# Optimization experiments

Measured on AMD Instinct MI355X. Metric: run time of the kernel, lower is better.

Reference implementation:

```python
import jax, jax.numpy as jnp
import numpy as np

HIDDEN = 128

def _conv1d(x, w, b):
    # x: [B, Cin, W], w: [Cout, Cin, K] (OIW), 'same' padding
    pad = w.shape[-1] // 2
    y = jax.lax.conv_general_dilated(
        x, w, window_strides=(1,), padding=[(pad, pad)],
        dimension_numbers=('NCH', 'OIH', 'NCH'))
    return y + b[None, :, None]

def setup_inputs() -> dict:
    key = jax.random.key(0)
    k1, k2, k3 = jax.random.split(key, 3)
    B, T, C, W = 16, 64, 64, 256
    K = 5
    fan_in = (C + HIDDEN) * K
    x = jax.random.normal(k1, (B, T, C, W), dtype=jnp.float32)
    W_conv = jax.random.normal(k2, (4 * HIDDEN, C + HIDDEN, K), dtype=jnp.float32) / np.sqrt(fan_in)
    b_conv = jax.random.normal(k3, (4 * HIDDEN,), dtype=jnp.float32) * 0.01
    return {"x": x, "W_conv": W_conv, "b_conv": b_conv}

def reference(x, W_conv, b_conv):
    B, T, C, W = x.shape
    h0 = jnp.zeros((B, HIDDEN, W), dtype=x.dtype)
    c0 = jnp.zeros((B, HIDDEN, W), dtype=x.dtype)

    def step(carry, xt):
        h, c = carry
        combined = jnp.concatenate([xt, h], axis=1)  # [B, C+H, W]
        conv_out = _conv1d(combined, W_conv, b_conv)  # [B, 4H, W]
        cc_i, cc_f, cc_o, cc_g = jnp.split(conv_out, 4, axis=1)
        i = jax.nn.sigmoid(cc_i)
        f = jax.nn.sigmoid(cc_f)
        o = jax.nn.sigmoid(cc_o)
        g = jnp.tanh(cc_g)
        c_next = f * c + i * g
        h_next = o * jnp.tanh(c_next)
        return (h_next, c_next), h_next

    xs = jnp.transpose(x, (1, 0, 2, 3))  # [T, B, C, W]
    (h, c), hs = jax.lax.scan(step, (h0, c0), xs)
    outputs = jnp.transpose(hs, (1, 0, 2, 3))  # [B, T, H, W]
    return outputs, h, c
```

## Files before the change

kernel.cpp:

```cpp
#include <hip/hip_runtime.h>
#include <hip/hip_bf16.h>
#include <math.h>

#define B_ 16
#define T_ 64
#define C_ 64
#define W_ 256
#define H_ 128
#define CH_ 192
#define K_ 5

#define OUT_SEQ_ELEMS ((size_t)B_ * T_ * H_ * W_)
#define OUT_H_OFF     OUT_SEQ_ELEMS
#define OUT_C_OFF     (OUT_SEQ_ELEMS + (size_t)B_ * H_ * W_)

#define WS_WF_OFF  0
#define WS_XT_OFF  (983040)
#define WS_HT_OFF  (WS_XT_OFF + 33554432)
#define WS_CNT_OFF (WS_HT_OFF + 2 * 1048576)

typedef __attribute__((ext_vector_type(8))) short bf16x8;
typedef __attribute__((ext_vector_type(4))) float f32x4;
typedef __attribute__((ext_vector_type(4))) unsigned int u32x4;

__device__ __forceinline__ float sigmoid_f(float x) {
    return 1.0f / (1.0f + __expf(-x));
}
__device__ __forceinline__ float tanh_f(float x) {
    return 1.0f - 2.0f / (__expf(2.0f * x) + 1.0f);
}

__global__ __launch_bounds__(256)
void prep_wfrag(const float* __restrict__ Wc, __hip_bfloat16* __restrict__ wf) {
    int idx = blockIdx.x * 256 + threadIdx.x;
    if (idx >= 960 * 64) return;
    int lane  = idx & 63;
    int f     = idx >> 6;
    int chunk = f % 6;
    int ktap  = (f / 6) % 5;
    int g     = (f / 30) % 4;
    int ht    = f / 120;
    int chan  = g * 128 + ht * 16 + (lane & 15);
    int ci0   = chunk * 32 + 8 * (lane >> 4);
    __hip_bfloat16 tmp[8];
#pragma unroll
    for (int j = 0; j < 8; ++j)
        tmp[j] = __float2bfloat16(Wc[((size_t)chan * CH_ + (ci0 + j)) * K_ + ktap]);
    *reinterpret_cast<u32x4*>(&wf[(size_t)idx * 8]) = *reinterpret_cast<const u32x4*>(tmp);
}

__global__ __launch_bounds__(256)
void prep_xt(const float* __restrict__ x, __hip_bfloat16* __restrict__ xt) {
    __shared__ float tile[64][65];
    int bt = blockIdx.x;
    int w0 = blockIdx.y * 64;
    const float* src = x + (size_t)bt * C_ * W_ + w0;
#pragma unroll
    for (int i = 0; i < 16; ++i) {
        int idx = i * 256 + threadIdx.x;
        int ci = idx >> 6, wr = idx & 63;
        tile[ci][wr] = src[(size_t)ci * W_ + wr];
    }
    __syncthreads();
    __hip_bfloat16* dst = xt + ((size_t)bt * W_ + w0) * C_;
#pragma unroll
    for (int i = 0; i < 8; ++i) {
        int idx = i * 256 + threadIdx.x;
        int wr = idx >> 5, cp = (idx & 31) * 2;
        __hip_bfloat16 a = __float2bfloat16(tile[cp][wr]);
        __hip_bfloat16 b = __float2bfloat16(tile[cp + 1][wr]);
        ushort2 v;
        v.x = *reinterpret_cast<unsigned short*>(&a);
        v.y = *reinterpret_cast<unsigned short*>(&b);
        *reinterpret_cast<ushort2*>(&dst[(size_t)wr * C_ + cp]) = v;
    }
}

__global__ void init_cnt(unsigned int* cnt) {
    if (threadIdx.x < 16 * 16) cnt[threadIdx.x] = 0;
}

#define PITCH_B 384
#define NROWS   132
#define GBUF_OFF 50688
#define HBF_OFF  (50688 + 32768)

__global__ __launch_bounds__(256, 1)
void lstm_persistent(const __hip_bfloat16* __restrict__ xt,
                     const __hip_bfloat16* __restrict__ wf,
                     const float* __restrict__ bc,
                     __hip_bfloat16* __restrict__ hbuf0,
                     __hip_bfloat16* __restrict__ hbuf1,
                     float* __restrict__ out,
                     unsigned int* __restrict__ cnt)
{
    __shared__ char lds[89600];
    const int ht   = blockIdx.x;
    const int wseg = blockIdx.y;
    const int b    = blockIdx.z;
    const int tid  = threadIdx.x;
    const int lane = tid & 63;
    const int g    = tid >> 6;
    const int l15  = lane & 15;
    const int lg   = lane >> 4;
    unsigned int* cntb = cnt + b * 16;

    bf16x8 wreg[30];
    {
        const __hip_bfloat16* wfbase = wf + (size_t)(ht * 4 + g) * 30 * 512 + (size_t)lane * 8;
#pragma unroll
        for (int f = 0; f < 30; ++f)
            wreg[f] = *reinterpret_cast<const bf16x8*>(wfbase + (size_t)f * 512);
    }
    float bias[4];
    {
        int chanbase = g * 128 + ht * 16 + (lg << 2);
#pragma unroll
        for (int r = 0; r < 4; ++r) bias[r] = bc[chanbase + r];
    }
    float cstate[8];
#pragma unroll
    for (int i = 0; i < 8; ++i) cstate[i] = 0.0f;

    const int wbase = wseg * 128 - 2;
    const int cib = 16 * lg;

    for (int idx = tid; idx < NROWS * 16; idx += 256) {
        int wrel = idx >> 4;
        int c16  = (idx & 15) + 8;
        int byteoff = wrel * PITCH_B + ((c16 * 16) ^ ((wrel & 7) << 4));
        u32x4 z = {0u, 0u, 0u, 0u};
        *reinterpret_cast<u32x4*>(lds + byteoff) = z;
    }

    for (int t = 0; t < T_; ++t) {
        const __hip_bfloat16* xrow = xt + ((size_t)(b * T_ + t) * W_) * C_;
        const __hip_bfloat16* hrow = ((t & 1) ? hbuf0 : hbuf1) + (size_t)b * W_ * H_;
        __hip_bfloat16* hout = ((t & 1) ? hbuf1 : hbuf0);

        for (int idx = tid; idx < NROWS * 8; idx += 256) {
            int wrel = idx >> 3;
            int c16  = idx & 7;
            int w = wbase + wrel;
            u32x4 v = {0u, 0u, 0u, 0u};
            if (w >= 0 && w < W_)
                v = *reinterpret_cast<const u32x4*>(xrow + (size_t)w * C_ + c16 * 8);
            int byteoff = wrel * PITCH_B + ((c16 * 16) ^ ((wrel & 7) << 4));
            *reinterpret_cast<u32x4*>(lds + byteoff) = v;
        }

        if (t > 0) {
            if (tid == 0) {
                unsigned int target = 16u * (unsigned int)t;
                while (__hip_atomic_load(cntb, __ATOMIC_RELAXED, __HIP_MEMORY_SCOPE_AGENT) < target)
                    __builtin_amdgcn_s_sleep(1);
            }
        }
        __syncthreads();
        __atomic_signal_fence(__ATOMIC_SEQ_CST);

        u32x4 hv[8];
        u32x4 hv8 = {0u, 0u, 0u, 0u};
        if (t > 0) {
            const u32x4 zz = {0u, 0u, 0u, 0u};
#pragma unroll
            for (int i = 0; i < 8; ++i) {
                int idx  = i * 256 + tid;
                int wrel = idx >> 4;
                int c16  = idx & 15;
                int w = wbase + wrel;
                hv[i] = zz;
                if (w >= 0 && w < W_) {
                    const __hip_bfloat16* hp = hrow + (size_t)w * H_ + c16 * 8;
                    asm volatile("global_load_dwordx4 %0, %1, off sc1"
                                 : "+v"(hv[i]) : "v"(hp));
                }
            }
            if (tid < 64) {
                int idx  = 2048 + tid;
                int wrel = idx >> 4;
                int c16  = idx & 15;
                int w = wbase + wrel;
                if (w >= 0 && w < W_) {
                    const __hip_bfloat16* hp = hrow + (size_t)w * H_ + c16 * 8;
                    asm volatile("global_load_dwordx4 %0, %1, off sc1"
                                 : "+v"(hv8) : "v"(hp));
                }
            }
        }

        f32x4 acc[8];
#pragma unroll
        for (int nf = 0; nf < 8; ++nf) {
            acc[nf][0] = bias[0]; acc[nf][1] = bias[1];
            acc[nf][2] = bias[2]; acc[nf][3] = bias[3];
        }
#pragma unroll
        for (int c = 0; c < 2; ++c) {
#pragma unroll
            for (int k = 0; k < K_; ++k) {
                bf16x8 afrag = wreg[k * 6 + c];
#pragma unroll
                for (int nf = 0; nf < 8; ++nf) {
                    int wrel = nf * 16 + l15 + k;
                    int byteoff = wrel * PITCH_B + ((c * 64 + cib) ^ ((wrel & 7) << 4));
                    bf16x8 bfrag = *reinterpret_cast<const bf16x8*>(lds + byteoff);
                    acc[nf] = __builtin_amdgcn_mfma_f32_16x16x32_bf16(afrag, bfrag, acc[nf], 0, 0, 0);
                }
            }
        }

        if (t > 0) {
            asm volatile("s_waitcnt vmcnt(0)" ::: "memory");
            __builtin_amdgcn_sched_barrier(0);
#pragma unroll
            for (int i = 0; i < 8; ++i) {
                int idx  = i * 256 + tid;
                int wrel = idx >> 4;
                int c16  = (idx & 15) + 8;
                int byteoff = wrel * PITCH_B + ((c16 * 16) ^ ((wrel & 7) << 4));
                *reinterpret_cast<u32x4*>(lds + byteoff) = hv[i];
            }
            if (tid < 64) {
                int idx  = 2048 + tid;
                int wrel = idx >> 4;
                int c16  = (idx & 15) + 8;
                int byteoff = wrel * PITCH_B + ((c16 * 16) ^ ((wrel & 7) << 4));
                *reinterpret_cast<u32x4*>(lds + byteoff) = hv8;
            }
        }
        __syncthreads();

#pragma unroll
        for (int c = 2; c < 6; ++c) {
#pragma unroll
            for (int k = 0; k < K_; ++k) {
                bf16x8 afrag = wreg[k * 6 + c];
#pragma unroll
                for (int nf = 0; nf < 8; ++nf) {
                    int wrel = nf * 16 + l15 + k;
                    int byteoff = wrel * PITCH_B + ((c * 64 + cib) ^ ((wrel & 7) << 4));
                    bf16x8 bfrag = *reinterpret_cast<const bf16x8*>(lds + byteoff);
                    acc[nf] = __builtin_amdgcn_mfma_f32_16x16x32_bf16(afrag, bfrag, acc[nf], 0, 0, 0);
                }
            }
        }

        float* gbuf = reinterpret_cast<float*>(lds + GBUF_OFF);
        {
            int rowb = lg << 2;
#pragma unroll
            for (int nf = 0; nf < 8; ++nf)
#pragma unroll
                for (int r = 0; r < 4; ++r)
                    gbuf[(g * 16 + rowb + r) * 128 + nf * 16 + l15] = acc[nf][r];
        }
        __syncthreads();

        __hip_bfloat16* hbf = reinterpret_cast<__hip_bfloat16*>(lds + HBF_OFF);
        float hn_r[8];
#pragma unroll
        for (int i = 0; i < 8; ++i) {
            int idx  = i * 256 + tid;
            int chan = idx >> 7;
            int pos  = idx & 127;
            float vi = gbuf[(0 * 16 + chan) * 128 + pos];
            float vf = gbuf[(1 * 16 + chan) * 128 + pos];
            float vo = gbuf[(2 * 16 + chan) * 128 + pos];
            float vg = gbuf[(3 * 16 + chan) * 128 + pos];
            float ii = sigmoid_f(vi), ff = sigmoid_f(vf), oo = sigmoid_f(vo), gg = tanh_f(vg);
            float cn = ff * cstate[i] + ii * gg;
            cstate[i] = cn;
            float hn = oo * tanh_f(cn);
            hn_r[i] = hn;
            hbf[pos * 24 + chan] = __float2bfloat16(hn);
        }
        __syncthreads();

        {
            int w = tid >> 1, grp = tid & 1;
            u32x4 v = *reinterpret_cast<const u32x4*>(lds + HBF_OFF + w * 48 + grp * 16);
            __hip_bfloat16* hp = hout + ((size_t)b * W_ + wseg * 128 + w) * H_ + ht * 16 + grp * 8;
            asm volatile("global_store_dwordx4 %0, %1, off sc1" :: "v"(hp), "v"(v) : "memory");
        }
        asm volatile("s_waitcnt vmcnt(0)" ::: "memory");
        __syncthreads();
        if (tid == 0)
            __hip_atomic_fetch_add(cntb, 1u, __ATOMIC_RELAXED, __HIP_MEMORY_SCOPE_AGENT);

        float* hw = out + ((size_t)(b * T_ + t) * H_ + ht * 16) * W_ + wseg * 128;
#pragma unroll
        for (int i = 0; i < 8; ++i) {
            int idx  = i * 256 + tid;
            int chan = idx >> 7;
            int pos  = idx & 127;
            hw[(size_t)chan * W_ + pos] = hn_r[i];
        }
        if (t == T_ - 1) {
#pragma unroll
            for (int i = 0; i < 8; ++i) {
                int idx  = i * 256 + tid;
                int chan = idx >> 7;
                int pos  = idx & 127;
                out[OUT_H_OFF + ((size_t)b * H_ + ht * 16 + chan) * W_ + wseg * 128 + pos] = hn_r[i];
                out[OUT_C_OFF + ((size_t)b * H_ + ht * 16 + chan) * W_ + wseg * 128 + pos] = cstate[i];
            }
        }
    }
}

extern "C" void kernel_launch(void* const* d_in, const int* in_sizes, int n_in,
                              void* d_out, int out_size, void* d_ws, size_t ws_size,
                              hipStream_t stream)
{
    const float* x  = (const float*)d_in[0];
    const float* Wc = (const float*)d_in[1];
    const float* bc = (const float*)d_in[2];
    float* out = (float*)d_out;
    char*  ws  = (char*)d_ws;

    __hip_bfloat16* wf  = (__hip_bfloat16*)(ws + WS_WF_OFF);
    __hip_bfloat16* xt  = (__hip_bfloat16*)(ws + WS_XT_OFF);
    __hip_bfloat16* hb0 = (__hip_bfloat16*)(ws + WS_HT_OFF);
    __hip_bfloat16* hb1 = (__hip_bfloat16*)(ws + WS_HT_OFF + 1048576);
    unsigned int*   cnt = (unsigned int*)(ws + WS_CNT_OFF);

    prep_wfrag<<<240, 256, 0, stream>>>(Wc, wf);
    prep_xt<<<dim3(B_ * T_, 4), 256, 0, stream>>>(x, xt);
    init_cnt<<<1, 256, 0, stream>>>(cnt);

    lstm_persistent<<<dim3(8, 2, B_), 256, 0, stream>>>(xt, wf, bc, hb0, hb1, out, cnt);
}
```

Baseline: 791.8 us.

## Split warps by gate pair and width half; prefetch next x-step into separate LDS region

Each warp now owns two gates and half of the width positions instead of one gate across all positions, so each B-fragment loaded from LDS feeds two MFMAs. This halves LDS fragment reads per MFMA, at the cost of twice as many weight registers (60 bf16x8 fragments per thread). The x and h tiles move to separate LDS regions with their own pitches. The next timestep's x tile is loaded while the kernel waits on the inter-block h barrier, taking the x load off the critical path. The extra register pressure risks spills or lower scheduling freedom.

```diff
diff --git a/kernel.cpp b/kernel.cpp
--- a/kernel.cpp
+++ b/kernel.cpp
@@ -80,8 +80,11 @@
     if (threadIdx.x < 16 * 16) cnt[threadIdx.x] = 0;
 }
 
-#define PITCH_B 384
 #define NROWS   132
+#define XPITCH  128
+#define HPITCH  256
+#define XOFF    0
+#define HOFF    16896
 #define GBUF_OFF 50688
 #define HBF_OFF  (50688 + 32768)
 
@@ -100,23 +103,28 @@
     const int b    = blockIdx.z;
     const int tid  = threadIdx.x;
     const int lane = tid & 63;
-    const int g    = tid >> 6;
+    const int wid  = tid >> 6;
+    const int gp   = wid & 1;
+    const int nh   = wid >> 1;
     const int l15  = lane & 15;
     const int lg   = lane >> 4;
     unsigned int* cntb = cnt + b * 16;
 
-    bf16x8 wreg[30];
-    {
-        const __hip_bfloat16* wfbase = wf + (size_t)(ht * 4 + g) * 30 * 512 + (size_t)lane * 8;
+    bf16x8 wreg[2][30];
+#pragma unroll
+    for (int gl = 0; gl < 2; ++gl) {
+        const __hip_bfloat16* wfbase =
+            wf + (size_t)(ht * 4 + 2 * gp + gl) * 30 * 512 + (size_t)lane * 8;
 #pragma unroll
         for (int f = 0; f < 30; ++f)
-            wreg[f] = *reinterpret_cast<const bf16x8*>(wfbase + (size_t)f * 512);
-    }
-    float bias[4];
-    {
-        int chanbase = g * 128 + ht * 16 + (lg << 2);
-#pragma unroll
-        for (int r = 0; r < 4; ++r) bias[r] = bc[chanbase + r];
+            wreg[gl][f] = *reinterpret_cast<const bf16x8*>(wfbase + (size_t)f * 512);
+    }
+    float bias[2][4];
+#pragma unroll
+    for (int gl = 0; gl < 2; ++gl) {
+        int chanbase = (2 * gp + gl) * 128 + ht * 16 + (lg << 2);
+#pragma unroll
+        for (int r = 0; r < 4; ++r) bias[gl][r] = bc[chanbase + r];
     }
     float cstate[8];
 #pragma unroll
@@ -125,28 +133,70 @@
     const int wbase = wseg * 128 - 2;
     const int cib = 16 * lg;
 
-    for (int idx = tid; idx < NROWS * 16; idx += 256) {
-        int wrel = idx >> 4;
-        int c16  = (idx & 15) + 8;
-        int byteoff = wrel * PITCH_B + ((c16 * 16) ^ ((wrel & 7) << 4));
-        u32x4 z = {0u, 0u, 0u, 0u};
-        *reinterpret_cast<u32x4*>(lds + byteoff) = z;
-    }
-
-    for (int t = 0; t < T_; ++t) {
-        const __hip_bfloat16* xrow = xt + ((size_t)(b * T_ + t) * W_) * C_;
-        const __hip_bfloat16* hrow = ((t & 1) ? hbuf0 : hbuf1) + (size_t)b * W_ * H_;
-        __hip_bfloat16* hout = ((t & 1) ? hbuf1 : hbuf0);
-
+    {
+        const __hip_bfloat16* xrow0 = xt + ((size_t)(b * T_ + 0) * W_) * C_;
         for (int idx = tid; idx < NROWS * 8; idx += 256) {
             int wrel = idx >> 3;
             int c16  = idx & 7;
             int w = wbase + wrel;
             u32x4 v = {0u, 0u, 0u, 0u};
             if (w >= 0 && w < W_)
-                v = *reinterpret_cast<const u32x4*>(xrow + (size_t)w * C_ + c16 * 8);
-            int byteoff = wrel * PITCH_B + ((c16 * 16) ^ ((wrel & 7) << 4));
+                v = *reinterpret_cast<const u32x4*>(xrow0 + (size_t)w * C_ + c16 * 8);
+            int byteoff = XOFF + wrel * XPITCH + ((c16 * 16) ^ ((wrel & 7) << 4));
             *reinterpret_cast<u32x4*>(lds + byteoff) = v;
+        }
+        for (int idx = tid; idx < NROWS * 16; idx += 256) {
+            int wrel = idx >> 4;
+            int slot = idx & 15;
+            int byteoff = HOFF + wrel * HPITCH + ((slot * 16) ^ ((wrel & 7) << 4));
+            u32x4 z = {0u, 0u, 0u, 0u};
+            *reinterpret_cast<u32x4*>(lds + byteoff) = z;
+        }
+    }
+    __syncthreads();
+
+    for (int t = 0; t < T_; ++t) {
+        const __hip_bfloat16* hrow = ((t & 1) ? hbuf0 : hbuf1) + (size_t)b * W_ * H_;
+        __hip_bfloat16* hout = ((t & 1) ? hbuf1 : hbuf0);
+
+        f32x4 acc[2][4];
+#pragma unroll
+        for (int gl = 0; gl < 2; ++gl)
+#pragma unroll
+            for (int nf = 0; nf < 4; ++nf) {
+                acc[gl][nf][0] = bias[gl][0]; acc[gl][nf][1] = bias[gl][1];
+                acc[gl][nf][2] = bias[gl][2]; acc[gl][nf][3] = bias[gl][3];
+            }
+#pragma unroll
+        for (int c = 0; c < 2; ++c)
+#pragma unroll
+            for (int k = 0; k < K_; ++k) {
+#pragma unroll
+                for (int nf = 0; nf < 4; ++nf) {
+                    int wrel = (nh * 4 + nf) * 16 + l15 + k;
+                    int byteoff = XOFF + wrel * XPITCH +
+                                  ((c * 64 + cib) ^ ((wrel & 7) << 4));
+                    bf16x8 bfrag = *reinterpret_cast<const bf16x8*>(lds + byteoff);
+                    acc[0][nf] = __builtin_amdgcn_mfma_f32_16x16x32_bf16(
+                        wreg[0][k * 6 + c], bfrag, acc[0][nf], 0, 0, 0);
+                    acc[1][nf] = __builtin_amdgcn_mfma_f32_16x16x32_bf16(
+                        wreg[1][k * 6 + c], bfrag, acc[1][nf], 0, 0, 0);
+                }
+            }
+        __syncthreads();
+
+        if (t + 1 < T_) {
+            const __hip_bfloat16* xrow = xt + ((size_t)(b * T_ + t + 1) * W_) * C_;
+            for (int idx = tid; idx < NROWS * 8; idx += 256) {
+                int wrel = idx >> 3;
+                int c16  = idx & 7;
+                int w = wbase + wrel;
+                u32x4 v = {0u, 0u, 0u, 0u};
+                if (w >= 0 && w < W_)
+                    v = *reinterpret_cast<const u32x4*>(xrow + (size_t)w * C_ + c16 * 8);
+                int byteoff = XOFF + wrel * XPITCH + ((c16 * 16) ^ ((wrel & 7) << 4));
+                *reinterpret_cast<u32x4*>(lds + byteoff) = v;
+            }
         }
 
         if (t > 0) {
@@ -159,19 +209,19 @@
         __syncthreads();
         __atomic_signal_fence(__ATOMIC_SEQ_CST);
 
-        u32x4 hv[8];
-        u32x4 hv8 = {0u, 0u, 0u, 0u};
         if (t > 0) {
+            u32x4 hv[8];
+            u32x4 hv8 = {0u, 0u, 0u, 0u};
             const u32x4 zz = {0u, 0u, 0u, 0u};
 #pragma unroll
             for (int i = 0; i < 8; ++i) {
                 int idx  = i * 256 + tid;
                 int wrel = idx >> 4;
-                int c16  = idx & 15;
+                int slot = idx & 15;
                 int w = wbase + wrel;
                 hv[i] = zz;
                 if (w >= 0 && w < W_) {
-                    const __hip_bfloat16* hp = hrow + (size_t)w * H_ + c16 * 8;
+                    const __hip_bfloat16* hp = hrow + (size_t)w * H_ + slot * 8;
                     asm volatile("global_load_dwordx4 %0, %1, off sc1"
                                  : "+v"(hv[i]) : "v"(hp));
                 }
@@ -179,81 +229,65 @@
             if (tid < 64) {
                 int idx  = 2048 + tid;
                 int wrel = idx >> 4;
-                int c16  = idx & 15;
+                int slot = idx & 15;
                 int w = wbase + wrel;
                 if (w >= 0 && w < W_) {
-                    const __hip_bfloat16* hp = hrow + (size_t)w * H_ + c16 * 8;
+                    const __hip_bfloat16* hp = hrow + (size_t)w * H_ + slot * 8;
                     asm volatile("global_load_dwordx4 %0, %1, off sc1"
                                  : "+v"(hv8) : "v"(hp));
                 }
             }
-        }
-
-        f32x4 acc[8];
-#pragma unroll
-        for (int nf = 0; nf < 8; ++nf) {
-            acc[nf][0] = bias[0]; acc[nf][1] = bias[1];
-            acc[nf][2] = bias[2]; acc[nf][3] = bias[3];
-        }
-#pragma unroll
-        for (int c = 0; c < 2; ++c) {
-#pragma unroll
-            for (int k = 0; k < K_; ++k) {
-                bf16x8 afrag = wreg[k * 6 + c];
-#pragma unroll
-                for (int nf = 0; nf < 8; ++nf) {
-                    int wrel = nf * 16 + l15 + k;
-                    int byteoff = wrel * PITCH_B + ((c * 64 + cib) ^ ((wrel & 7) << 4));
-                    bf16x8 bfrag = *reinterpret_cast<const bf16x8*>(lds + byteoff);
-                    acc[nf] = __builtin_amdgcn_mfma_f32_16x16x32_bf16(afrag, bfrag, acc[nf], 0, 0, 0);
-                }
-            }
-        }
-
-        if (t > 0) {
             asm volatile("s_waitcnt vmcnt(0)" ::: "memory");
             __builtin_amdgcn_sched_barrier(0);
 #pragma unroll
             for (int i = 0; i < 8; ++i) {
                 int idx  = i * 256 + tid;
                 int wrel = idx >> 4;
-                int c16  = (idx & 15) + 8;
-                int byteoff = wrel * PITCH_B + ((c16 * 16) ^ ((wrel & 7) << 4));
+                int slot = idx & 15;
+                int byteoff = HOFF + wrel * HPITCH + ((slot * 16) ^ ((wrel & 7) << 4));
                 *reinterpret_cast<u32x4*>(lds + byteoff) = hv[i];
             }
             if (tid < 64) {
                 int idx  = 2048 + tid;
                 int wrel = idx >> 4;
-                int c16  = (idx & 15) + 8;
-                int byteoff = wrel * PITCH_B + ((c16 * 16) ^ ((wrel & 7) << 4));
+                int slot = idx & 15;
+                int byteoff = HOFF + wrel * HPITCH + ((slot * 16) ^ ((wrel & 7) << 4));
                 *reinterpret_cast<u32x4*>(lds + byteoff) = hv8;
             }
         }
         __syncthreads();
 
 #pragma unroll
-        for (int c = 2; c < 6; ++c) {
+        for (int c = 2; c < 6; ++c)
 #pragma unroll
             for (int k = 0; k < K_; ++k) {
-                bf16x8 afrag = wreg[k * 6 + c];
-#pragma unroll
-                for (int nf = 0; nf < 8; ++nf) {
-                    int wrel = nf * 16 + l15 + k;
-                    int byteoff = wrel * PITCH_B + ((c * 64 + cib) ^ ((wrel & 7) << 4));
+#pragma unroll
+                for (int nf = 0; nf < 4; ++nf) {
+                    int wrel = (nh * 4 + nf) * 16 + l15 + k;
+                    int byteoff = HOFF + wrel * HPITCH +
+                                  (((c - 2) * 64 + cib) ^ ((wrel & 7) << 4));
                     bf16x8 bfrag = *reinterpret_cast<const bf16x8*>(lds + byteoff);
-                    acc[nf] = __builtin_amdgcn_mfma_f32_16x16x32_bf16(afrag, bfrag, acc[nf], 0, 0, 0);
-                }
-            }
-        }
+                    acc[0][nf] = __builtin_amdgcn_mfma_f32_16x16x32_bf16(
+                        wreg[0][k * 6 + c], bfrag, acc[0][nf], 0, 0, 0);
+                    acc[1][nf] = __builtin_amdgcn_mfma_f32_16x16x32_bf16(
+                        wreg[1][k * 6 + c], bfrag, acc[1][nf], 0, 0, 0);
+                }
+            }
 
         float* gbuf = reinterpret_cast<float*>(lds + GBUF_OFF);
         {
             int rowb = lg << 2;
 #pragma unroll
-            for (int nf = 0; nf < 8; ++nf)
-#pragma unroll
-                for (int r = 0; r < 4; ++r)
-                    gbuf[(g * 16 + rowb + r) * 128 + nf * 16 + l15] = acc[nf][r];
+            for (int gl = 0; gl < 2; ++gl) {
+                int grow = (2 * gp + gl) * 16 + rowb;
+#pragma unroll
+                for (int nf = 0; nf < 4; ++nf) {
+                    int col = (nh * 4 + nf) * 16 + l15;
+#pragma unroll
+                    for (int r = 0; r < 4; ++r)
+                        gbuf[(grow + r) * 128 + col] = acc[gl][nf][r];
+                }
+            }
         }
         __syncthreads();
 
```

New measurement: 816.3 us. 1.03x slower.

## Replace atomic counter barrier with per-block flag slots and register-packed h store

Applied to the files above, without the earlier changes.

Each block now publishes its completed timestep to its own padded flag slot instead of incrementing a shared per-batch counter. Waiters poll all 16 slots in parallel across a wavefront. The gate epilogue is remapped so each thread owns 8 channels at one position, which lets it pack bf16 h values in registers and store them directly, removing the LDS staging buffer and one __syncthreads. The gate buffer also gets an XOR swizzle to cut LDS bank conflicts. The cost is that each thread's fp32 output writes now stride across channels.

```diff
diff --git a/kernel.cpp b/kernel.cpp
--- a/kernel.cpp
+++ b/kernel.cpp
@@ -77,13 +77,13 @@
 }
 
 __global__ void init_cnt(unsigned int* cnt) {
-    if (threadIdx.x < 16 * 16) cnt[threadIdx.x] = 0;
+    cnt[blockIdx.x * 256 + threadIdx.x] = 0;
 }
 
 #define PITCH_B 384
 #define NROWS   132
 #define GBUF_OFF 50688
-#define HBF_OFF  (50688 + 32768)
+#define GIDX2(row, col) ((row) * 128 + ((col) ^ ((((row) >> 2) & 3) << 4)))
 
 __global__ __launch_bounds__(256, 1)
 void lstm_persistent(const __hip_bfloat16* __restrict__ xt,
@@ -92,18 +92,19 @@
                      __hip_bfloat16* __restrict__ hbuf0,
                      __hip_bfloat16* __restrict__ hbuf1,
                      float* __restrict__ out,
-                     unsigned int* __restrict__ cnt)
+                     unsigned int* __restrict__ slots)
 {
-    __shared__ char lds[89600];
+    __shared__ char lds[83456];
     const int ht   = blockIdx.x;
     const int wseg = blockIdx.y;
     const int b    = blockIdx.z;
+    const int hw16 = ht * 2 + wseg;
     const int tid  = threadIdx.x;
     const int lane = tid & 63;
     const int g    = tid >> 6;
     const int l15  = lane & 15;
     const int lg   = lane >> 4;
-    unsigned int* cntb = cnt + b * 16;
+    unsigned int* slotb = slots + (size_t)b * 256;
 
     bf16x8 wreg[30];
     {
@@ -118,12 +119,11 @@
 #pragma unroll
         for (int r = 0; r < 4; ++r) bias[r] = bc[chanbase + r];
     }
+    const int epos = tid & 127;
+    const int ehi  = tid >> 7;
     float cstate[8];
 #pragma unroll
     for (int i = 0; i < 8; ++i) cstate[i] = 0.0f;
-
-    const int wbase = wseg * 128 - 2;
-    const int cib = 16 * lg;
 
     for (int idx = tid; idx < NROWS * 16; idx += 256) {
         int wrel = idx >> 4;
@@ -132,6 +132,9 @@
         u32x4 z = {0u, 0u, 0u, 0u};
         *reinterpret_cast<u32x4*>(lds + byteoff) = z;
     }
+
+    const int wbase = wseg * 128 - 2;
+    const int cib = 16 * lg;
 
     for (int t = 0; t < T_; ++t) {
         const __hip_bfloat16* xrow = xt + ((size_t)(b * T_ + t) * W_) * C_;
@@ -149,12 +152,12 @@
             *reinterpret_cast<u32x4*>(lds + byteoff) = v;
         }
 
-        if (t > 0) {
-            if (tid == 0) {
-                unsigned int target = 16u * (unsigned int)t;
-                while (__hip_atomic_load(cntb, __ATOMIC_RELAXED, __HIP_MEMORY_SCOPE_AGENT) < target)
-                    __builtin_amdgcn_s_sleep(1);
-            }
+        if (t > 0 && tid < 64) {
+            unsigned int tgt = (unsigned int)t;
+            const unsigned int* sp = slotb + (lane & 15) * 16;
+            while (!__all(__hip_atomic_load(sp, __ATOMIC_RELAXED,
+                                            __HIP_MEMORY_SCOPE_AGENT) >= tgt))
+                __builtin_amdgcn_s_sleep(1);
         }
         __syncthreads();
         __atomic_signal_fence(__ATOMIC_SEQ_CST);
@@ -167,11 +170,11 @@
             for (int i = 0; i < 8; ++i) {
                 int idx  = i * 256 + tid;
                 int wrel = idx >> 4;
-                int c16  = idx & 15;
+                int slot = idx & 15;
                 int w = wbase + wrel;
                 hv[i] = zz;
                 if (w >= 0 && w < W_) {
-                    const __hip_bfloat16* hp = hrow + (size_t)w * H_ + c16 * 8;
+                    const __hip_bfloat16* hp = hrow + (size_t)w * H_ + slot * 8;
                     asm volatile("global_load_dwordx4 %0, %1, off sc1"
                                  : "+v"(hv[i]) : "v"(hp));
                 }
@@ -179,10 +182,10 @@
             if (tid < 64) {
                 int idx  = 2048 + tid;
                 int wrel = idx >> 4;
-                int c16  = idx & 15;
+                int slot = idx & 15;
                 int w = wbase + wrel;
                 if (w >= 0 && w < W_) {
-                    const __hip_bfloat16* hp = hrow + (size_t)w * H_ + c16 * 8;
+                    const __hip_bfloat16* hp = hrow + (size_t)w * H_ + slot * 8;
                     asm volatile("global_load_dwordx4 %0, %1, off sc1"
                                  : "+v"(hv8) : "v"(hp));
                 }
@@ -252,58 +255,54 @@
 #pragma unroll
             for (int nf = 0; nf < 8; ++nf)
 #pragma unroll
-                for (int r = 0; r < 4; ++r)
-                    gbuf[(g * 16 + rowb + r) * 128 + nf * 16 + l15] = acc[nf][r];
+                for (int r = 0; r < 4; ++r) {
+                    int row = g * 16 + rowb + r;
+                    gbuf[GIDX2(row, nf * 16 + l15)] = acc[nf][r];
+                }
         }
         __syncthreads();
 
-        __hip_bfloat16* hbf = reinterpret_cast<__hip_bfloat16*>(lds + HBF_OFF);
-        float hn_r[8];
-#pragma unroll
-        for (int i = 0; i < 8; ++i) {
-            int idx  = i * 256 + tid;
-            int chan = idx >> 7;
-            int pos  = idx & 127;
-            float vi = gbuf[(0 * 16 + chan) * 128 + pos];
-            float vf = gbuf[(1 * 16 + chan) * 128 + pos];
-            float vo = gbuf[(2 * 16 + chan) * 128 + pos];
-            float vg = gbuf[(3 * 16 + chan) * 128 + pos];
-            float ii = sigmoid_f(vi), ff = sigmoid_f(vf), oo = sigmoid_f(vo), gg = tanh_f(vg);
-            float cn = ff * cstate[i] + ii * gg;
-            cstate[i] = cn;
+        float hn8[8];
+        unsigned int pk[4] = {0u, 0u, 0u, 0u};
+#pragma unroll
+        for (int j = 0; j < 8; ++j) {
+            int chan = ehi * 8 + j;
+            float vi = gbuf[GIDX2(0 * 16 + chan, epos)];
+            float vf = gbuf[GIDX2(1 * 16 + chan, epos)];
+            float vo = gbuf[GIDX2(2 * 16 + chan, epos)];
+            float vg = gbuf[GIDX2(3 * 16 + chan, epos)];
+            float ii = sigmoid_f(vi), ff = sigmoid_f(vf);
+            float oo = sigmoid_f(vo), gg = tanh_f(vg);
+            float cn = ff * cstate[j] + ii * gg;
+            cstate[j] = cn;
             float hn = oo * tanh_f(cn);
-            hn_r[i] = hn;
-            hbf[pos * 24 + chan] = __float2bfloat16(hn);
-        }
-        __syncthreads();
+            hn8[j] = hn;
+            __hip_bfloat16 hb = __float2bfloat16(hn);
+            pk[j >> 1] |= ((unsigned int)*reinterpret_cast<unsigned short*>(&hb)) << (16 * (j & 1));
+        }
+        u32x4 pv = { pk[0], pk[1], pk[2], pk[3] };
 
         {
-            int w = tid >> 1, grp = tid & 1;
-            u32x4 v = *reinterpret_cast<const u32x4*>(lds + HBF_OFF + w * 48 + grp * 16);
-            __hip_bfloat16* hp = hout + ((size_t)b * W_ + wseg * 128 + w) * H_ + ht * 16 + grp * 8;
-            asm volatile("global_store_dwordx4 %0, %1, off sc1" :: "v"(hp), "v"(v) : "memory");
+            __hip_bfloat16* hp = hout + ((size_t)b * W_ + wseg * 128 + epos) * H_
+                                      + ht * 16 + ehi * 8;
+            asm volatile("global_store_dwordx4 %0, %1, off sc1" :: "v"(hp), "v"(pv) : "memory");
         }
         asm volatile("s_waitcnt vmcnt(0)" ::: "memory");
         __syncthreads();
         if (tid == 0)
-            __hip_atomic_fetch_add(cntb, 1u, __ATOMIC_RELAXED, __HIP_MEMORY_SCOPE_AGENT);
+            __hip_atomic_store(slotb + hw16 * 16, (unsigned int)(t + 1),
+                               __ATOMIC_RELAXED, __HIP_MEMORY_SCOPE_AGENT);
 
         float* hw = out + ((size_t)(b * T_ + t) * H_ + ht * 16) * W_ + wseg * 128;
 #pragma unroll
-        for (int i = 0; i < 8; ++i) {
-            int idx  = i * 256 + tid;
-            int chan = idx >> 7;
-            int pos  = idx & 127;
-            hw[(size_t)chan * W_ + pos] = hn_r[i];
-        }
+        for (int j = 0; j < 8; ++j)
+            hw[(size_t)(ehi * 8 + j) * W_ + epos] = hn8[j];
         if (t == T_ - 1) {
 #pragma unroll
-            for (int i = 0; i < 8; ++i) {
-                int idx  = i * 256 + tid;
-                int chan = idx >> 7;
-                int pos  = idx & 127;
-                out[OUT_H_OFF + ((size_t)b * H_ + ht * 16 + chan) * W_ + wseg * 128 + pos] = hn_r[i];
-                out[OUT_C_OFF + ((size_t)b * H_ + ht * 16 + chan) * W_ + wseg * 128 + pos] = cstate[i];
+            for (int j = 0; j < 8; ++j) {
+                size_t base = ((size_t)b * H_ + ht * 16 + ehi * 8 + j) * W_ + wseg * 128 + epos;
+                out[OUT_H_OFF + base] = hn8[j];
+                out[OUT_C_OFF + base] = cstate[j];
             }
         }
     }
@@ -327,7 +326,7 @@
 
     prep_wfrag<<<240, 256, 0, stream>>>(Wc, wf);
     prep_xt<<<dim3(B_ * T_, 4), 256, 0, stream>>>(x, xt);
-    init_cnt<<<1, 256, 0, stream>>>(cnt);
+    init_cnt<<<16, 256, 0, stream>>>(cnt);
 
     lstm_persistent<<<dim3(8, 2, B_), 256, 0, stream>>>(xt, wf, bc, hb0, hb1, out, cnt);
 }
```

Measured after the change: 785.3 us (median of 2 runs). Within noise of the previous version (-0.8%).
